# Performance work log

Measured on AMD Instinct MI355X. Metric: run time of the kernel, lower is better.

## Reference

```python
import jax, jax.numpy as jnp
import numpy as np

WEIGHT_BITS = 8
INPUT_BITS = 8
HIDDEN = 4096
INTERMEDIATE = 16384
CLIP_INIT = 2.5


def _sym_quantize(x, clip_val, num_bits):
    """Symmetric layerwise uniform quantization with STE (PACT-style clip).

    Forward: clamp to [-clip, clip], round to 2^(b-1)-1 levels, dequantize.
    """
    clip_val = jnp.abs(clip_val)
    x_c = jnp.clip(x, -clip_val, clip_val)
    scale = clip_val / (2 ** (num_bits - 1) - 1)
    q = jnp.round(x_c / scale) * scale
    # straight-through estimator: gradient flows through the clamp only
    return x_c + jax.lax.stop_gradient(q - x_c)


def setup_inputs() -> dict:
    key = jax.random.key(0)
    k1, k2, k3 = jax.random.split(key, 3)
    hidden_states = jax.random.normal(k1, (2, 2048, HIDDEN), dtype=jnp.float32)
    # nn.Linear default init scale ~ 1/sqrt(fan_in)
    weight = jax.random.normal(k2, (INTERMEDIATE, HIDDEN), dtype=jnp.float32) / np.sqrt(HIDDEN)
    bias = jax.random.normal(k3, (INTERMEDIATE,), dtype=jnp.float32) * 0.01
    weight_clip_val = jnp.float32(CLIP_INIT)
    input_clip_val = jnp.float32(CLIP_INIT)
    return {
        "hidden_states": hidden_states,
        "weight": weight,
        "bias": bias,
        "weight_clip_val": weight_clip_val,
        "input_clip_val": input_clip_val,
    }


def reference(hidden_states, weight, bias, weight_clip_val, input_clip_val):
    wq = _sym_quantize(weight, weight_clip_val, WEIGHT_BITS)        # [I, H]
    xq = _sym_quantize(hidden_states, input_clip_val, INPUT_BITS)   # [B, S, H]
    out = jnp.einsum("bsh,ih->bsi", xq, wq) + bias                  # [B, S, I]
    return jax.nn.relu(out)
```

## Files before the change

kernel.cpp:

```cpp
#include <hip/hip_runtime.h>


#define HIDDEN 4096
#define INTER 16384
#define MDIM 4096
#define BK 128
#define NT (HIDDEN / BK)

typedef int v4i __attribute__((ext_vector_type(4)));

__global__ __launch_bounds__(256) void quantize_kernel(
    const float* __restrict__ x,
    signed char* __restrict__ q,
    const float* __restrict__ clip_ptr,
    int n4)
{
    int i = blockIdx.x * blockDim.x + threadIdx.x;
    if (i >= n4) return;
    float c = fabsf(clip_ptr[0]);
    float inv_scale = 127.0f / c;
    float4 v = reinterpret_cast<const float4*>(x)[i];
    int q0 = __float2int_rn(fminf(fmaxf(v.x, -c), c) * inv_scale);
    int q1 = __float2int_rn(fminf(fmaxf(v.y, -c), c) * inv_scale);
    int q2 = __float2int_rn(fminf(fmaxf(v.z, -c), c) * inv_scale);
    int q3 = __float2int_rn(fminf(fmaxf(v.w, -c), c) * inv_scale);
    int pack = (q0 & 0xff) | ((q1 & 0xff) << 8) | ((q2 & 0xff) << 16) | (q3 << 24);
    reinterpret_cast<int*>(q)[i] = pack;
}

__global__ __launch_bounds__(256) void quantize_pack_b_kernel(
    const float* __restrict__ x,
    signed char* __restrict__ qp,
    const float* __restrict__ clip_ptr,
    int n4)
{
    int i = blockIdx.x * blockDim.x + threadIdx.x;
    if (i >= n4) return;
    float c = fabsf(clip_ptr[0]);
    float inv_scale = 127.0f / c;
    float4 v = reinterpret_cast<const float4*>(x)[i];
    int q0 = __float2int_rn(fminf(fmaxf(v.x, -c), c) * inv_scale);
    int q1 = __float2int_rn(fminf(fmaxf(v.y, -c), c) * inv_scale);
    int q2 = __float2int_rn(fminf(fmaxf(v.z, -c), c) * inv_scale);
    int q3 = __float2int_rn(fminf(fmaxf(v.w, -c), c) * inv_scale);
    int pack = (q0 & 0xff) | ((q1 & 0xff) << 8) | ((q2 & 0xff) << 16) | (q3 << 24);
    int n = i >> 10;
    int k = (i & 1023) << 2;
    size_t addr = ((size_t)(n >> 4) << 16) | ((size_t)(k >> 6) << 10)
                | ((size_t)((k >> 4) & 3) << 8) | ((size_t)(n & 15) << 4)
                | (size_t)(k & 15);
    *reinterpret_cast<int*>(qp + addr) = pack;
}


#define GLL(src, dst) __builtin_amdgcn_global_load_lds( \
    (const __attribute__((address_space(1))) void*)(src), \
    (__attribute__((address_space(3))) void*)(dst), 16, 0, 0)

#define STAGE(gptr, lptr) do { \
    GLL((gptr), (lptr)); \
    GLL((gptr) + (size_t)64 * HIDDEN, (lptr) + 8192); } while (0)

#define BARX() __builtin_amdgcn_s_barrier()
#define LGKM0() asm volatile("s_waitcnt lgkmcnt(0)" ::: "memory")
#define VM12() asm volatile("s_waitcnt vmcnt(12)" ::: "memory")
#define VM8() asm volatile("s_waitcnt vmcnt(8)" ::: "memory")
#define VMNOP()
#define PRIO1() __builtin_amdgcn_s_setprio(1)
#define PRIO0() __builtin_amdgcn_s_setprio(0)

#define READ_A(cb, qm) do { _Pragma("unroll") \
    for (int m_ = 0; m_ < 4; m_++) { \
      const signed char* p_ = &As[cb][(qm) * 16384 + aOff + m_ * 2048]; \
      a[m_][0] = *reinterpret_cast<const v4i*>(p_ + c0); \
      a[m_][1] = *reinterpret_cast<const v4i*>(p_ + c1); } } while (0)

#define LOADB(dst, qn, kf0) do { _Pragma("unroll") \
    for (int n_ = 0; n_ < 2; n_++) { _Pragma("unroll") \
      for (int kk_ = 0; kk_ < 2; kk_++) { \
        dst[n_][kk_] = *reinterpret_cast<const v4i*>( \
            bpw + (((size_t)((qn) * 8 + n_) << 16) | \
                   ((size_t)((kf0) + kk_) << 10)) + L16); } } } while (0)

#define MFMA_Q(qm, qn, bset) do { _Pragma("unroll") \
    for (int m_ = 0; m_ < 4; m_++) { _Pragma("unroll") \
      for (int n_ = 0; n_ < 2; n_++) \
        acc[qm][qn][m_][n_] = __builtin_amdgcn_mfma_i32_16x16x64_i8( \
            a[m_][0], bset[n_][0], acc[qm][qn][m_][n_], 0, 0, 0); } \
    _Pragma("unroll") \
    for (int m_ = 0; m_ < 4; m_++) { _Pragma("unroll") \
      for (int n_ = 0; n_ < 2; n_++) \
        acc[qm][qn][m_][n_] = __builtin_amdgcn_mfma_i32_16x16x64_i8( \
            a[m_][1], bset[n_][1], acc[qm][qn][m_][n_], 0, 0, 0); } } while (0)

#define GROUP(cb, T, S2, SB, VMW) do { \
     \
    READ_A(cb, 0); \
    LOADB(b1, 1, (T) * 2); \
    BARX(); LGKM0(); PRIO1(); MFMA_Q(0, 0, b0); PRIO0(); BARX(); \
     \
    if (S2) STAGE(gA + (size_t)((T) + 2) * BK, &As[cb][0] + ldsT); \
    BARX(); PRIO1(); MFMA_Q(0, 1, b1); PRIO0(); BARX(); \
     \
    READ_A(cb, 1); \
    BARX(); LGKM0(); PRIO1(); MFMA_Q(1, 0, b0); PRIO0(); BARX(); \
     \
    if (SB) LOADB(b0, 0, ((T) + 1) * 2); \
    if (S2) STAGE(gA + (size_t)128 * HIDDEN + (size_t)((T) + 2) * BK, \
                  &As[cb][16384] + ldsT); \
    VMW(); \
    BARX(); PRIO1(); MFMA_Q(1, 1, b1); PRIO0(); BARX(); \
  } while (0)

__global__ __launch_bounds__(512, 2) void gemm_i8_kernel(
    const signed char* __restrict__ qA,
    const signed char* __restrict__ Bp,
    const float* __restrict__ bias,
    const float* __restrict__ wclip,
    const float* __restrict__ iclip,
    float* __restrict__ out)
{
    __shared__ __align__(16) signed char As[2][32768];

    const int t = threadIdx.x;
    const int L = t & 63;
    const int W = t >> 6;
    const int wm = W >> 2;
    const int wn = W & 3;
    const int lane16 = L & 15;
    const int quad = L >> 4;
    const int swz = lane16 & 7;
    const int L16 = L * 16;

    int wg = blockIdx.y * 64 + blockIdx.x;
    wg = (wg & 7) * 128 + (wg >> 3);
    const int mBase = (wg >> 6) * 256;
    const int nBase = (wg & 63) * 256;

    const int sRow = t >> 3;
    const int sColSwz = ((t & 7) ^ (sRow & 7)) * 16;
    const signed char* gA = qA + (size_t)(mBase + sRow) * HIDDEN + sColSwz;
    const int ldsT = t * 16;

    const int aOff = (wm * 64 + lane16) * 128;
    const int c0 = (quad ^ swz) * 16;
    const int c1 = ((quad + 4) ^ swz) * 16;

    const signed char* bpw = Bp + ((size_t)((nBase >> 4) + wn * 2) << 16);

    v4i acc[2][2][4][2];
#pragma unroll
    for (int i = 0; i < 2; i++)
#pragma unroll
        for (int j = 0; j < 2; j++)
#pragma unroll
            for (int m = 0; m < 4; m++)
#pragma unroll
                for (int n = 0; n < 2; n++)
                    acc[i][j][m][n] = (v4i){0, 0, 0, 0};

    v4i a[4][2], b0[2][2], b1[2][2];

    STAGE(gA, &As[0][0] + ldsT);
    STAGE(gA + (size_t)128 * HIDDEN, &As[0][16384] + ldsT);
    STAGE(gA + BK, &As[1][0] + ldsT);
    STAGE(gA + (size_t)128 * HIDDEN + BK, &As[1][16384] + ldsT);
    LOADB(b0, 0, 0);
    VM8();
    BARX();

    for (int T = 0; T < NT - 2; T += 2) {
        GROUP(0, T,     1, 1, VM12);
        GROUP(1, T + 1, 1, 1, VM12);
    }
    GROUP(0, NT - 2, 0, 1, VM8);
    GROUP(1, NT - 1, 0, 0, VMNOP);

    const float scale = (fabsf(wclip[0]) / 127.0f) * (fabsf(iclip[0]) / 127.0f);

    float bv[2][2];
#pragma unroll
    for (int qn = 0; qn < 2; qn++)
#pragma unroll
        for (int n = 0; n < 2; n++)
            bv[qn][n] = bias[nBase + qn * 128 + wn * 32 + n * 16 + lane16];

#pragma unroll
    for (int qm = 0; qm < 2; qm++)
#pragma unroll
        for (int m = 0; m < 4; m++)
#pragma unroll
            for (int r = 0; r < 4; r++) {
                const int row = mBase + qm * 128 + wm * 64 + m * 16 + quad * 4 + r;
                float* orow = out + (size_t)row * INTER + nBase + wn * 32 + lane16;
#pragma unroll
                for (int qn = 0; qn < 2; qn++)
#pragma unroll
                    for (int n = 0; n < 2; n++) {
                        float v = (float)acc[qm][qn][m][n][r] * scale + bv[qn][n];
                        orow[qn * 128 + n * 16] = fmaxf(v, 0.0f);
                    }
            }
}

extern "C" void kernel_launch(void* const* d_in, const int* in_sizes, int n_in,
                              void* d_out, int out_size, void* d_ws, size_t ws_size,
                              hipStream_t stream) {
    const float* hidden_states  = (const float*)d_in[0];
    const float* weight         = (const float*)d_in[1];
    const float* bias           = (const float*)d_in[2];
    const float* weight_clip    = (const float*)d_in[3];
    const float* input_clip     = (const float*)d_in[4];
    float* out = (float*)d_out;

    signed char* qA = (signed char*)d_ws;
    signed char* Bp = qA + (size_t)MDIM * HIDDEN;

    {
        int n4 = MDIM * HIDDEN / 4;
        quantize_kernel<<<n4 / 256, 256, 0, stream>>>(hidden_states, qA, input_clip, n4);
    }
    {
        int n4 = INTER * HIDDEN / 4;
        quantize_pack_b_kernel<<<n4 / 256, 256, 0, stream>>>(weight, Bp, weight_clip, n4);
    }

    dim3 grid(INTER / 256, MDIM / 256);
    gemm_i8_kernel<<<grid, 512, 0, stream>>>(qA, Bp, bias, weight_clip, input_clip, out);
}
```

Measured before the change: 752.7 us.

## Halve GEMM M-tile to 128 with 4 waves; pack B with 16-byte writes

The int8 GEMM block tile shrinks from 256x256 with 8 waves to 128x256 with 4 waves. LDS drops to 32KB, the grid doubles and the workgroup swizzle is adjusted to match. The weight quantize-pack kernel now has each thread handle 16 consecutive k values and write one 16-byte vector instead of 4-byte scattered stores, which cuts store transactions. The smaller tile lowers A reuse per B load, so B traffic doubles and there are more blocks to schedule, in exchange for possibly better occupancy and latency hiding.

```diff
diff --git a/kernel.cpp b/kernel.cpp
--- a/kernel.cpp
+++ b/kernel.cpp
@@ -32,24 +32,28 @@
     const float* __restrict__ x,
     signed char* __restrict__ qp,
     const float* __restrict__ clip_ptr,
-    int n4)
+    int n16)
 {
     int i = blockIdx.x * blockDim.x + threadIdx.x;
-    if (i >= n4) return;
+    if (i >= n16) return;
     float c = fabsf(clip_ptr[0]);
     float inv_scale = 127.0f / c;
-    float4 v = reinterpret_cast<const float4*>(x)[i];
-    int q0 = __float2int_rn(fminf(fmaxf(v.x, -c), c) * inv_scale);
-    int q1 = __float2int_rn(fminf(fmaxf(v.y, -c), c) * inv_scale);
-    int q2 = __float2int_rn(fminf(fmaxf(v.z, -c), c) * inv_scale);
-    int q3 = __float2int_rn(fminf(fmaxf(v.w, -c), c) * inv_scale);
-    int pack = (q0 & 0xff) | ((q1 & 0xff) << 8) | ((q2 & 0xff) << 16) | (q3 << 24);
-    int n = i >> 10;
-    int k = (i & 1023) << 2;
+    int n = i >> 8;
+    int k = (i & 255) << 4;
+    const float4* src = reinterpret_cast<const float4*>(x + (size_t)n * HIDDEN + k);
+    int pk[4];
+#pragma unroll
+    for (int j = 0; j < 4; j++) {
+        float4 v = src[j];
+        int q0 = __float2int_rn(fminf(fmaxf(v.x, -c), c) * inv_scale);
+        int q1 = __float2int_rn(fminf(fmaxf(v.y, -c), c) * inv_scale);
+        int q2 = __float2int_rn(fminf(fmaxf(v.z, -c), c) * inv_scale);
+        int q3 = __float2int_rn(fminf(fmaxf(v.w, -c), c) * inv_scale);
+        pk[j] = (q0 & 0xff) | ((q1 & 0xff) << 8) | ((q2 & 0xff) << 16) | (q3 << 24);
+    }
     size_t addr = ((size_t)(n >> 4) << 16) | ((size_t)(k >> 6) << 10)
-                | ((size_t)((k >> 4) & 3) << 8) | ((size_t)(n & 15) << 4)
-                | (size_t)(k & 15);
-    *reinterpret_cast<int*>(qp + addr) = pack;
+                | ((size_t)((k >> 4) & 3) << 8) | ((size_t)(n & 15) << 4);
+    *reinterpret_cast<v4i*>(qp + addr) = *reinterpret_cast<v4i*>(pk);
 }
 
 
@@ -57,9 +61,9 @@
     (const __attribute__((address_space(1))) void*)(src), \
     (__attribute__((address_space(3))) void*)(dst), 16, 0, 0)
 
-#define STAGE(gptr, lptr) do { \
+#define STAGE_HALF(gptr, lptr) do { \
     GLL((gptr), (lptr)); \
-    GLL((gptr) + (size_t)64 * HIDDEN, (lptr) + 8192); } while (0)
+    GLL((gptr) + (size_t)32 * HIDDEN, (lptr) + 4096); } while (0)
 
 #define BARX() __builtin_amdgcn_s_barrier()
 #define LGKM0() asm volatile("s_waitcnt lgkmcnt(0)" ::: "memory")
@@ -71,7 +75,7 @@
 
 #define READ_A(cb, qm) do { _Pragma("unroll") \
     for (int m_ = 0; m_ < 4; m_++) { \
-      const signed char* p_ = &As[cb][(qm) * 16384 + aOff + m_ * 2048]; \
+      const signed char* p_ = &As[cb][(qm) * 8192 + aOff + m_ * 2048]; \
       a[m_][0] = *reinterpret_cast<const v4i*>(p_ + c0); \
       a[m_][1] = *reinterpret_cast<const v4i*>(p_ + c1); } } while (0)
 
@@ -99,20 +103,20 @@
     LOADB(b1, 1, (T) * 2); \
     BARX(); LGKM0(); PRIO1(); MFMA_Q(0, 0, b0); PRIO0(); BARX(); \
      \
-    if (S2) STAGE(gA + (size_t)((T) + 2) * BK, &As[cb][0] + ldsT); \
+    if (S2) STAGE_HALF(gA + (size_t)((T) + 2) * BK, &As[cb][0] + ldsT); \
     BARX(); PRIO1(); MFMA_Q(0, 1, b1); PRIO0(); BARX(); \
      \
     READ_A(cb, 1); \
     BARX(); LGKM0(); PRIO1(); MFMA_Q(1, 0, b0); PRIO0(); BARX(); \
      \
     if (SB) LOADB(b0, 0, ((T) + 1) * 2); \
-    if (S2) STAGE(gA + (size_t)128 * HIDDEN + (size_t)((T) + 2) * BK, \
-                  &As[cb][16384] + ldsT); \
+    if (S2) STAGE_HALF(gA + (size_t)64 * HIDDEN + (size_t)((T) + 2) * BK, \
+                       &As[cb][8192] + ldsT); \
     VMW(); \
     BARX(); PRIO1(); MFMA_Q(1, 1, b1); PRIO0(); BARX(); \
   } while (0)
 
-__global__ __launch_bounds__(512, 2) void gemm_i8_kernel(
+__global__ __launch_bounds__(256, 2) void gemm_i8_kernel(
     const signed char* __restrict__ qA,
     const signed char* __restrict__ Bp,
     const float* __restrict__ bias,
@@ -120,21 +124,20 @@
     const float* __restrict__ iclip,
     float* __restrict__ out)
 {
-    __shared__ __align__(16) signed char As[2][32768];
+    __shared__ __align__(16) signed char As[2][16384];
 
     const int t = threadIdx.x;
     const int L = t & 63;
     const int W = t >> 6;
-    const int wm = W >> 2;
-    const int wn = W & 3;
+    const int wn = W;
     const int lane16 = L & 15;
     const int quad = L >> 4;
     const int swz = lane16 & 7;
     const int L16 = L * 16;
 
     int wg = blockIdx.y * 64 + blockIdx.x;
-    wg = (wg & 7) * 128 + (wg >> 3);
-    const int mBase = (wg >> 6) * 256;
+    wg = (wg & 7) * 256 + (wg >> 3);
+    const int mBase = (wg >> 6) * 128;
     const int nBase = (wg & 63) * 256;
 
     const int sRow = t >> 3;
@@ -142,7 +145,7 @@
     const signed char* gA = qA + (size_t)(mBase + sRow) * HIDDEN + sColSwz;
     const int ldsT = t * 16;
 
-    const int aOff = (wm * 64 + lane16) * 128;
+    const int aOff = lane16 * 128;
     const int c0 = (quad ^ swz) * 16;
     const int c1 = ((quad + 4) ^ swz) * 16;
 
@@ -161,10 +164,10 @@
 
     v4i a[4][2], b0[2][2], b1[2][2];
 
-    STAGE(gA, &As[0][0] + ldsT);
-    STAGE(gA + (size_t)128 * HIDDEN, &As[0][16384] + ldsT);
-    STAGE(gA + BK, &As[1][0] + ldsT);
-    STAGE(gA + (size_t)128 * HIDDEN + BK, &As[1][16384] + ldsT);
+    STAGE_HALF(gA,                              &As[0][0]    + ldsT);
+    STAGE_HALF(gA + (size_t)64 * HIDDEN,        &As[0][8192] + ldsT);
+    STAGE_HALF(gA + BK,                         &As[1][0]    + ldsT);
+    STAGE_HALF(gA + (size_t)64 * HIDDEN + BK,   &As[1][8192] + ldsT);
     LOADB(b0, 0, 0);
     VM8();
     BARX();
@@ -191,7 +194,7 @@
         for (int m = 0; m < 4; m++)
 #pragma unroll
             for (int r = 0; r < 4; r++) {
-                const int row = mBase + qm * 128 + wm * 64 + m * 16 + quad * 4 + r;
+                const int row = mBase + qm * 64 + m * 16 + quad * 4 + r;
                 float* orow = out + (size_t)row * INTER + nBase + wn * 32 + lane16;
 #pragma unroll
                 for (int qn = 0; qn < 2; qn++)
@@ -221,10 +224,10 @@
         quantize_kernel<<<n4 / 256, 256, 0, stream>>>(hidden_states, qA, input_clip, n4);
     }
     {
-        int n4 = INTER * HIDDEN / 4;
-        quantize_pack_b_kernel<<<n4 / 256, 256, 0, stream>>>(weight, Bp, weight_clip, n4);
-    }
-
-    dim3 grid(INTER / 256, MDIM / 256);
-    gemm_i8_kernel<<<grid, 512, 0, stream>>>(qA, Bp, bias, weight_clip, input_clip, out);
-}
+        int n16 = INTER * HIDDEN / 16;
+        quantize_pack_b_kernel<<<n16 / 256, 256, 0, stream>>>(weight, Bp, weight_clip, n16);
+    }
+
+    dim3 grid(INTER / 256, MDIM / 128);
+    gemm_i8_kernel<<<grid, 256, 0, stream>>>(qA, Bp, bias, weight_clip, input_clip, out);
+}
```

Result: slower. 813.5 us (+8.1%).
